# Kernel optimization log

Hardware: AMD Instinct MI355X
Metric: run time of the kernel (lower is better)

The kernel has to match this reference:

```python
import jax, jax.numpy as jnp
import numpy as np

N_HEADS = 16
HEAD_SIZE = 64
D_EMBD = 1024
BLOCK_SIZE = 1024
B, T = 4, 1024


def setup_inputs() -> dict:
    key = jax.random.key(0)
    ks = jax.random.split(key, 6)
    s = 0.02
    x = jax.random.normal(ks[0], (B, T, D_EMBD), dtype=jnp.float32)
    # per-head bias-free Q/K/V projections, stacked: [H, C, Hs]
    Wq = jax.random.normal(ks[1], (N_HEADS, D_EMBD, HEAD_SIZE), dtype=jnp.float32) * s
    Wk = jax.random.normal(ks[2], (N_HEADS, D_EMBD, HEAD_SIZE), dtype=jnp.float32) * s
    Wv = jax.random.normal(ks[3], (N_HEADS, D_EMBD, HEAD_SIZE), dtype=jnp.float32) * s
    # output projection W_o: Linear(d_embd, d_embd) with bias
    Wo = jax.random.normal(ks[4], (D_EMBD, D_EMBD), dtype=jnp.float32) * s
    bo = jax.random.normal(ks[5], (D_EMBD,), dtype=jnp.float32) * s
    return {"x": x, "Wq": Wq, "Wk": Wk, "Wv": Wv, "Wo": Wo, "bo": bo}


def reference(x, Wq, Wk, Wv, Wo, bo):
    # Batched equivalent of the per-head loop: q,k,v: [B, H, T, Hs]
    q = jnp.einsum('btc,hcs->bhts', x, Wq)
    k = jnp.einsum('btc,hcs->bhts', x, Wk)
    v = jnp.einsum('btc,hcs->bhts', x, Wv)
    scale = 1.0 / jnp.sqrt(jnp.asarray(HEAD_SIZE, dtype=x.dtype))
    scores = jnp.einsum('bhts,bhus->bhtu', q, k) * scale  # [B,H,T,T]
    causal = jnp.tril(jnp.ones((T, T), dtype=bool))
    scores = jnp.where(causal[None, None, :, :], scores, jnp.asarray(-jnp.inf, dtype=x.dtype))
    wei = jax.nn.softmax(scores, axis=-1)  # dropout p=0.0 -> identity
    out = jnp.einsum('bhtu,bhus->bhts', wei, v)  # [B,H,T,Hs]
    out = out.transpose(0, 2, 1, 3).reshape(B, T, D_EMBD)  # concat heads
    return out @ Wo.T + bo  # final Linear; dropout p=0.0 -> identity
```

## Files before the change

kernel.cpp:

```cpp
#include <hip/hip_runtime.h>
#include <hip/hip_bf16.h>
#include <math.h>

#define NH 16
#define HS 64
#define DE 1024
#define TT 1024
#define BBATCH 4
#define MTOK 4096

typedef __bf16 v8bf __attribute__((ext_vector_type(8)));
typedef __bf16 v4bf __attribute__((ext_vector_type(4)));
typedef float  v4f  __attribute__((ext_vector_type(4)));

__device__ __forceinline__ void gl_lds16(const __bf16* g, __bf16* l) {
    __builtin_amdgcn_global_load_lds(
        (const __attribute__((address_space(1))) unsigned int*)g,
        (__attribute__((address_space(3))) unsigned int*)l, 16, 0, 0);
}

__global__ __launch_bounds__(256) void prep_all_kernel(
    const float* __restrict__ x,  __bf16* __restrict__ xb,
    const float* __restrict__ Wo, __bf16* __restrict__ Wob,
    const float* __restrict__ Wq, const float* __restrict__ Wk,
    const float* __restrict__ Wv, __bf16* __restrict__ Wt)
{
    const int bid = blockIdx.x;
    const int t = threadIdx.x;
    if (bid < 5120) {
        int i = bid * 256 + t;
        const float* in; __bf16* out;
        if (i < 1048576) { in = x;  out = xb; }
        else             { in = Wo; out = Wob; i -= 1048576; }
        float4 v = ((const float4*)in)[i];
        v4bf o;
        o[0] = (__bf16)v.x; o[1] = (__bf16)v.y; o[2] = (__bf16)v.z; o[3] = (__bf16)v.w;
        *(v4bf*)&out[(size_t)i * 4] = o;
        return;
    }
    const int bid2 = bid - 5120;
    const int c0 = (bid2 & 15) * 64, h = (bid2 >> 4) & 15, m = bid2 >> 8;
    const float* W = (m == 0) ? Wq : (m == 1) ? Wk : Wv;
    __shared__ float tile[64][65];
    #pragma unroll
    for (int pp = 0; pp < 16; ++pp) {
        int cl = pp * 4 + (t >> 6);
        int s  = t & 63;
        tile[cl][s] = W[((size_t)h * DE + c0 + cl) * HS + s];
    }
    __syncthreads();
    #pragma unroll
    for (int pp = 0; pp < 16; ++pp) {
        int s  = pp * 4 + (t >> 6);
        int cl = t & 63;
        Wt[((size_t)(m * DE + h * HS + s)) * DE + c0 + cl] = (__bf16)tile[cl][s];
    }
}

__device__ __forceinline__ void gemm_stage(
    const __bf16* __restrict__ Ab, const __bf16* __restrict__ Bb,
    __bf16* As, __bf16* Bs, int K, int k0, int w, int l)
{
    #pragma unroll
    for (int i = 0; i < 4; ++i) {
        int p   = i * 256 + w * 64 + l;
        int row = p >> 3;
        int lc  = (p & 7) ^ (row & 7);
        gl_lds16(Ab + (size_t)row * K + k0 + lc * 8, As + p * 8);
        gl_lds16(Bb + (size_t)row * K + k0 + lc * 8, Bs + p * 8);
    }
}

__global__ __launch_bounds__(256) void gemm_bt_kernel(
    const __bf16* __restrict__ A, const __bf16* __restrict__ Bt,
    int K,
    __bf16* __restrict__ qk_out, __bf16* __restrict__ vt_out)
{
    __shared__ __align__(16) __bf16 As[128 * 64];
    __shared__ __align__(16) __bf16 Bs[128 * 64];
    const int tid = threadIdx.x;
    const int w = tid >> 6, l = tid & 63;
    const int wm = w >> 1, wn = w & 1;
    const int lhi = l >> 4, llo = l & 15;
    const int sw0 = ((lhi ^ (llo & 7)) << 3);
    const int sw1 = sw0 ^ 32;

    const int lin = blockIdx.x;
    const int xcd = lin & 7, j = lin >> 3;
    const int bm = xcd * 4 + (j & 3);
    const int bn = j >> 2;

    v4f acc[4][4];
    #pragma unroll
    for (int i = 0; i < 4; ++i)
        #pragma unroll
        for (int jj = 0; jj < 4; ++jj)
            #pragma unroll
            for (int r = 0; r < 4; ++r) acc[i][jj][r] = 0.f;

    const __bf16* Ab = A  + (size_t)bm * 128 * K;
    const __bf16* Bb = Bt + (size_t)bn * 128 * K;

    const int niter = K >> 6;
    for (int it = 0; it < niter; ++it) {
        if (it) __syncthreads();
        gemm_stage(Ab, Bb, As, Bs, K, it * 64, w, l);
        __syncthreads();
        #pragma unroll
        for (int kk = 0; kk < 64; kk += 32) {
            const int sw = kk ? sw1 : sw0;
            v8bf a[4], b[4];
            #pragma unroll
            for (int i = 0; i < 4; ++i)
                a[i] = *(const v8bf*)&As[(wm * 64 + i * 16 + llo) * 64 + sw];
            #pragma unroll
            for (int jj = 0; jj < 4; ++jj)
                b[jj] = *(const v8bf*)&Bs[(wn * 64 + jj * 16 + llo) * 64 + sw];
            #pragma unroll
            for (int i = 0; i < 4; ++i)
                #pragma unroll
                for (int jj = 0; jj < 4; ++jj)
                    acc[i][jj] = __builtin_amdgcn_mfma_f32_16x16x32_bf16(a[i], b[jj], acc[i][jj], 0, 0, 0);
        }
    }

    const int row0 = bm * 128 + wm * 64;
    const int col0 = bn * 128 + wn * 64;

    if (col0 < 2048) {
        #pragma unroll
        for (int i = 0; i < 4; ++i) {
            int rbase = row0 + i * 16 + lhi * 4;
            #pragma unroll
            for (int jj = 0; jj < 4; ++jj) {
                int c = col0 + jj * 16 + llo;
                #pragma unroll
                for (int r = 0; r < 4; ++r)
                    qk_out[(size_t)(rbase + r) * 2048 + c] = (__bf16)acc[i][jj][r];
            }
        }
    } else {
        #pragma unroll
        for (int i = 0; i < 4; ++i) {
            int rbase = row0 + i * 16 + lhi * 4;
            int bidx = rbase >> 10, t0 = rbase & 1023;
            #pragma unroll
            for (int jj = 0; jj < 4; ++jj) {
                int c = col0 + jj * 16 + llo - 2048;
                v4bf pk;
                #pragma unroll
                for (int r = 0; r < 4; ++r) pk[r] = (__bf16)acc[i][jj][r];
                *(v4bf*)&vt_out[((size_t)(bidx * NH + (c >> 6)) * HS + (c & 63)) * TT + t0] = pk;
            }
        }
    }
}

__global__ __launch_bounds__(256) void gemm_bt64_kernel(
    const __bf16* __restrict__ A, const __bf16* __restrict__ Bt, int K,
    float* __restrict__ f_out, const float* __restrict__ bias)
{
    __shared__ __align__(16) __bf16 As[2][64 * 64];
    __shared__ __align__(16) __bf16 Bs[2][128 * 64];
    const int tid = threadIdx.x;
    const int w = tid >> 6, l = tid & 63;
    const int wm = w & 1, wn = w >> 1;
    const int lhi = l >> 4, llo = l & 15;
    const int sw0 = ((lhi ^ (llo & 7)) << 3);
    const int sw1 = sw0 ^ 32;

    const int lin = blockIdx.x;
    const int xcd = lin & 7, j = lin >> 3;
    const int bm = xcd * 8 + (j & 7);
    const int bn = j >> 3;

    v4f acc[2][4];
    #pragma unroll
    for (int i = 0; i < 2; ++i)
        #pragma unroll
        for (int jj = 0; jj < 4; ++jj)
            #pragma unroll
            for (int r = 0; r < 4; ++r) acc[i][jj][r] = 0.f;

    const __bf16* Ab = A  + (size_t)bm * 64 * K;
    const __bf16* Bb = Bt + (size_t)bn * 128 * K;

    const int niter = K >> 6;
    {
        #pragma unroll
        for (int i = 0; i < 2; ++i) {
            int p = i * 256 + tid, row = p >> 3, lc = (p & 7) ^ (row & 7);
            gl_lds16(Ab + (size_t)row * K + lc * 8, As[0] + p * 8);
        }
        #pragma unroll
        for (int i = 0; i < 4; ++i) {
            int p = i * 256 + tid, row = p >> 3, lc = (p & 7) ^ (row & 7);
            gl_lds16(Bb + (size_t)row * K + lc * 8, Bs[0] + p * 8);
        }
    }

    for (int it = 0; it < niter; ++it) {
        const int buf = it & 1;
        __syncthreads();
        if (it + 1 < niter) {
            const int k0 = (it + 1) * 64;
            #pragma unroll
            for (int i = 0; i < 2; ++i) {
                int p = i * 256 + tid, row = p >> 3, lc = (p & 7) ^ (row & 7);
                gl_lds16(Ab + (size_t)row * K + k0 + lc * 8, As[buf ^ 1] + p * 8);
            }
            #pragma unroll
            for (int i = 0; i < 4; ++i) {
                int p = i * 256 + tid, row = p >> 3, lc = (p & 7) ^ (row & 7);
                gl_lds16(Bb + (size_t)row * K + k0 + lc * 8, Bs[buf ^ 1] + p * 8);
            }
        }
        #pragma unroll
        for (int kk = 0; kk < 64; kk += 32) {
            const int sw = kk ? sw1 : sw0;
            v8bf a[2], b[4];
            #pragma unroll
            for (int i = 0; i < 2; ++i)
                a[i] = *(const v8bf*)&As[buf][(wm * 32 + i * 16 + llo) * 64 + sw];
            #pragma unroll
            for (int jj = 0; jj < 4; ++jj)
                b[jj] = *(const v8bf*)&Bs[buf][(wn * 64 + jj * 16 + llo) * 64 + sw];
            #pragma unroll
            for (int i = 0; i < 2; ++i)
                #pragma unroll
                for (int jj = 0; jj < 4; ++jj)
                    acc[i][jj] = __builtin_amdgcn_mfma_f32_16x16x32_bf16(a[i], b[jj], acc[i][jj], 0, 0, 0);
        }
    }

    const int row0 = bm * 64 + wm * 32;
    const int col0 = bn * 128 + wn * 64;
    #pragma unroll
    for (int jj = 0; jj < 4; ++jj) {
        int c = col0 + jj * 16 + llo;
        float bv = bias[c];
        #pragma unroll
        for (int i = 0; i < 2; ++i) {
            int rbase = row0 + i * 16 + lhi * 4;
            #pragma unroll
            for (int r = 0; r < 4; ++r)
                f_out[(size_t)(rbase + r) * DE + c] = acc[i][jj][r] + bv;
        }
    }
}

__device__ __forceinline__ v4f bf_mfma(v8bf a, v8bf b, v4f c) {
    return __builtin_amdgcn_mfma_f32_16x16x32_bf16(a, b, c, 0, 0, 0);
}

__device__ __forceinline__ void stage_kv(
    const __bf16* __restrict__ kb, const __bf16* __restrict__ vb,
    __bf16* Ksb, __bf16* Vsb, int k0, int tid)
{
    #pragma unroll
    for (int i = 0; i < 2; ++i) {
        int p   = i * 256 + tid;
        int row = p >> 3;
        int lc  = (p & 7) ^ (row & 7);
        gl_lds16(kb + (size_t)(k0 + row) * 2048 + lc * 8, Ksb + p * 8);
        gl_lds16(vb + (size_t)row * TT + k0 + lc * 8,     Vsb + p * 8);
    }
}

template<bool DIAG>
__device__ __forceinline__ void attn_compute(
    const __bf16* __restrict__ Ksb, const __bf16* __restrict__ Vsb,
    __bf16* __restrict__ PsW, int k0, int r0, int lhi, int llo, int sw0, int sw1,
    v8bf aq0, v8bf aq1, v4f (&o)[4], float (&l_part)[4])
{
    v4f sacc[4];
    #pragma unroll
    for (int n = 0; n < 4; ++n)
        #pragma unroll
        for (int r = 0; r < 4; ++r) sacc[n][r] = 0.f;
    #pragma unroll
    for (int n = 0; n < 4; ++n) {
        v8bf bk0 = *(const v8bf*)&Ksb[(n * 16 + llo) * 64 + sw0];
        v8bf bk1 = *(const v8bf*)&Ksb[(n * 16 + llo) * 64 + sw1];
        sacc[n] = bf_mfma(aq0, bk0, sacc[n]);
        sacc[n] = bf_mfma(aq1, bk1, sacc[n]);
    }

    float prob[4][4];
    #pragma unroll
    for (int n = 0; n < 4; ++n) {
        int colg = k0 + n * 16 + llo;
        #pragma unroll
        for (int r = 0; r < 4; ++r) {
            float s2 = sacc[n][r] * 0.18033688f;
            if (DIAG) { int rowg = r0 + lhi * 4 + r; if (colg > rowg) s2 = -1e30f; }
            float p = exp2f(s2);
            prob[n][r] = p;
            l_part[r] += p;
        }
    }

    #pragma unroll
    for (int r = 0; r < 4; ++r) {
        int prow = lhi * 4 + r;
        #pragma unroll
        for (int n = 0; n < 4; ++n) {
            int g = (n * 2 + (llo >> 3)) ^ (prow & 7);
            PsW[prow * 64 + g * 8 + (llo & 7)] = (__bf16)prob[n][r];
        }
    }

    #pragma unroll
    for (int kk = 0; kk < 64; kk += 32) {
        v8bf ap = *(const v8bf*)&PsW[llo * 64 + (((kk >> 3) + lhi) ^ (llo & 7)) * 8];
        const int sw = kk ? sw1 : sw0;
        #pragma unroll
        for (int n = 0; n < 4; ++n) {
            v8bf bv = *(const v8bf*)&Vsb[(n * 16 + llo) * 64 + sw];
            o[n] = bf_mfma(ap, bv, o[n]);
        }
    }
}

__global__ __launch_bounds__(256) void attn_kernel(
    const __bf16* __restrict__ qk, const __bf16* __restrict__ vt,
    __bf16* __restrict__ att)
{
    __shared__ __align__(16) __bf16 Ks[2][64 * 64];
    __shared__ __align__(16) __bf16 Vs[2][64 * 64];
    __shared__ __align__(16) __bf16 Ps[4][16 * 64];

    const int tid = threadIdx.x;
    const int w = tid >> 6, l = tid & 63;
    const int lhi = l >> 4, llo = l & 15;
    const int sw0 = ((lhi ^ (llo & 7)) << 3);
    const int sw1 = sw0 ^ 32;
    const int bh = blockIdx.x & 63;
    const int k = blockIdx.x >> 6;
    const int qt = (k & 4) ? (k >= 12 ? k - 12 : k + 4) : (15 - k);
    const int b = bh >> 4, h = bh & 15;

    const __bf16* qbase = qk + (size_t)b * TT * 2048 + h * HS;
    const __bf16* kbase = qk + (size_t)b * TT * 2048 + 1024 + h * HS;
    const __bf16* vbase = vt + (size_t)bh * HS * TT;
    __bf16* PsW = &Ps[w][0];

    const int r0 = qt * 64 + w * 16;

    stage_kv(kbase, vbase, Ks[0], Vs[0], 0, tid);

    v8bf aq0 = *(const v8bf*)&qbase[(size_t)(r0 + llo) * 2048 + lhi * 8];
    v8bf aq1 = *(const v8bf*)&qbase[(size_t)(r0 + llo) * 2048 + 32 + lhi * 8];

    float l_part[4] = {0.f, 0.f, 0.f, 0.f};
    v4f o[4];
    #pragma unroll
    for (int n = 0; n < 4; ++n)
        #pragma unroll
        for (int r = 0; r < 4; ++r) o[n][r] = 0.f;

    for (int kt = 0; kt < qt; ++kt) {
        const int buf = kt & 1;
        __syncthreads();
        stage_kv(kbase, vbase, Ks[buf ^ 1], Vs[buf ^ 1], (kt + 1) * 64, tid);
        attn_compute<false>(Ks[buf], Vs[buf], PsW, kt * 64, r0, lhi, llo, sw0, sw1, aq0, aq1, o, l_part);
    }
    __syncthreads();
    attn_compute<true>(Ks[qt & 1], Vs[qt & 1], PsW, qt * 64, r0, lhi, llo, sw0, sw1, aq0, aq1, o, l_part);

    #pragma unroll
    for (int r = 0; r < 4; ++r) {
        float s = l_part[r];
        #pragma unroll
        for (int msk = 1; msk < 16; msk <<= 1) s += __shfl_xor(s, msk, 64);
        float inv = 1.f / s;
        int rowg = b * TT + r0 + lhi * 4 + r;
        #pragma unroll
        for (int n = 0; n < 4; ++n)
            att[(size_t)rowg * DE + h * HS + n * 16 + llo] = (__bf16)(o[n][r] * inv);
    }
}

extern "C" void kernel_launch(void* const* d_in, const int* in_sizes, int n_in,
                              void* d_out, int out_size, void* d_ws, size_t ws_size,
                              hipStream_t stream)
{
    const float* x  = (const float*)d_in[0];
    const float* Wq = (const float*)d_in[1];
    const float* Wk = (const float*)d_in[2];
    const float* Wv = (const float*)d_in[3];
    const float* Wo = (const float*)d_in[4];
    const float* bo = (const float*)d_in[5];
    float* out = (float*)d_out;

    char* ws = (char*)d_ws;
    __bf16* xb  = (__bf16*)(ws);
    __bf16* Wt  = (__bf16*)(ws + 8388608);
    __bf16* Wob = (__bf16*)(ws + 14680064);
    __bf16* qk  = (__bf16*)(ws + 16777216);
    __bf16* vt  = (__bf16*)(ws + 33554432);
    __bf16* att = (__bf16*)(ws + 41943040);

    prep_all_kernel<<<5888, 256, 0, stream>>>(x, xb, Wo, Wob, Wq, Wk, Wv, Wt);
    gemm_bt_kernel<<<768, 256, 0, stream>>>(xb, Wt, 1024, qk, vt);
    attn_kernel<<<1024, 256, 0, stream>>>(qk, vt, att);
    gemm_bt64_kernel<<<512, 256, 0, stream>>>(att, Wob, 1024, out, bo);
}
```

Measured before the change: 156.5 us.

## Replace QKV GEMM with 256x256 double-buffered 8-phase pipelined kernel

Replaces the 128x128 single-buffered QKV projection GEMM with a 512-thread kernel that computes 256x256 tiles. It double-buffers A and B in LDS and splits each K step into four phases. Global-to-LDS loads for the next step are interleaved with MFMA work, using explicit vmcnt waits, raw s_barrier calls and setprio. The goal is to hide load latency and raise data reuse per block. In exchange, only 192 blocks are launched and each needs 128KB of LDS, so fewer blocks than CUs and one block per CU.

```diff
diff --git a/kernel.cpp b/kernel.cpp
--- a/kernel.cpp
+++ b/kernel.cpp
@@ -17,6 +17,16 @@
     __builtin_amdgcn_global_load_lds(
         (const __attribute__((address_space(1))) unsigned int*)g,
         (__attribute__((address_space(3))) unsigned int*)l, 16, 0, 0);
+}
+
+__device__ __forceinline__ v4f bf_mfma(v8bf a, v8bf b, v4f c) {
+    return __builtin_amdgcn_mfma_f32_16x16x32_bf16(a, b, c, 0, 0, 0);
+}
+
+__device__ __forceinline__ void wg_barrier() {
+    asm volatile("" ::: "memory");
+    __builtin_amdgcn_s_barrier();
+    asm volatile("" ::: "memory");
 }
 
 __global__ __launch_bounds__(256) void prep_all_kernel(
@@ -57,99 +67,152 @@
     }
 }
 
-__device__ __forceinline__ void gemm_stage(
-    const __bf16* __restrict__ Ab, const __bf16* __restrict__ Bb,
-    __bf16* As, __bf16* Bs, int K, int k0, int w, int l)
-{
-    #pragma unroll
-    for (int i = 0; i < 4; ++i) {
-        int p   = i * 256 + w * 64 + l;
-        int row = p >> 3;
-        int lc  = (p & 7) ^ (row & 7);
-        gl_lds16(Ab + (size_t)row * K + k0 + lc * 8, As + p * 8);
-        gl_lds16(Bb + (size_t)row * K + k0 + lc * 8, Bs + p * 8);
-    }
-}
-
-__global__ __launch_bounds__(256) void gemm_bt_kernel(
+__device__ __forceinline__ void stage_half(
+    const __bf16* __restrict__ Gb, __bf16* Ls, int h, int k0, int tid)
+{
+    #pragma unroll
+    for (int i = 0; i < 2; ++i) {
+        int p  = i * 512 + tid;
+        int r  = p >> 3;
+        int lc = (p & 7) ^ (r & 7);
+        gl_lds16(Gb + (size_t)(h * 128 + r) * 1024 + k0 + lc * 8, Ls + h * 128 * 64 + p * 8);
+    }
+}
+
+__global__ __launch_bounds__(512, 2) void gemm_qkv_8ph(
     const __bf16* __restrict__ A, const __bf16* __restrict__ Bt,
-    int K,
     __bf16* __restrict__ qk_out, __bf16* __restrict__ vt_out)
 {
-    __shared__ __align__(16) __bf16 As[128 * 64];
-    __shared__ __align__(16) __bf16 Bs[128 * 64];
+    __shared__ __align__(16) __bf16 As[2][256 * 64];
+    __shared__ __align__(16) __bf16 Bs[2][256 * 64];
     const int tid = threadIdx.x;
     const int w = tid >> 6, l = tid & 63;
-    const int wm = w >> 1, wn = w & 1;
+    const int wm = w >> 2, wn = w & 3;
     const int lhi = l >> 4, llo = l & 15;
     const int sw0 = ((lhi ^ (llo & 7)) << 3);
     const int sw1 = sw0 ^ 32;
 
     const int lin = blockIdx.x;
-    const int xcd = lin & 7, j = lin >> 3;
-    const int bm = xcd * 4 + (j & 3);
-    const int bn = j >> 2;
-
-    v4f acc[4][4];
-    #pragma unroll
-    for (int i = 0; i < 4; ++i)
-        #pragma unroll
-        for (int jj = 0; jj < 4; ++jj)
-            #pragma unroll
-            for (int r = 0; r < 4; ++r) acc[i][jj][r] = 0.f;
-
-    const __bf16* Ab = A  + (size_t)bm * 128 * K;
-    const __bf16* Bb = Bt + (size_t)bn * 128 * K;
-
-    const int niter = K >> 6;
-    for (int it = 0; it < niter; ++it) {
-        if (it) __syncthreads();
-        gemm_stage(Ab, Bb, As, Bs, K, it * 64, w, l);
-        __syncthreads();
-        #pragma unroll
-        for (int kk = 0; kk < 64; kk += 32) {
-            const int sw = kk ? sw1 : sw0;
-            v8bf a[4], b[4];
-            #pragma unroll
-            for (int i = 0; i < 4; ++i)
-                a[i] = *(const v8bf*)&As[(wm * 64 + i * 16 + llo) * 64 + sw];
-            #pragma unroll
-            for (int jj = 0; jj < 4; ++jj)
-                b[jj] = *(const v8bf*)&Bs[(wn * 64 + jj * 16 + llo) * 64 + sw];
-            #pragma unroll
-            for (int i = 0; i < 4; ++i)
+    const int xcd = lin & 7, chunk = lin >> 3;
+    const int bm = xcd * 2 + (chunk & 1);
+    const int bn = chunk >> 1;
+
+    const __bf16* Ab = A  + (size_t)bm * 256 * 1024;
+    const __bf16* Bb = Bt + (size_t)bn * 256 * 1024;
+
+    v4f acc[8][4];
+    #pragma unroll
+    for (int fr = 0; fr < 8; ++fr)
+        #pragma unroll
+        for (int fc = 0; fc < 4; ++fc)
+            #pragma unroll
+            for (int r = 0; r < 4; ++r) acc[fr][fc][r] = 0.f;
+
+    stage_half(Ab, (__bf16*)As[0], 0, 0, tid);
+    stage_half(Ab, (__bf16*)As[0], 1, 0, tid);
+    stage_half(Bb, (__bf16*)Bs[0], 0, 0, tid);
+    stage_half(Bb, (__bf16*)Bs[0], 1, 0, tid);
+    stage_half(Ab, (__bf16*)As[1], 0, 64, tid);
+    stage_half(Ab, (__bf16*)As[1], 1, 64, tid);
+    stage_half(Bb, (__bf16*)Bs[1], 0, 64, tid);
+
+    #pragma unroll 1
+    for (int t = 0; t < 16; ++t) {
+        const __bf16* Ap = As[t & 1];
+        const __bf16* Bp = Bs[t & 1];
+        __bf16* Anx = (__bf16*)As[(t & 1) ^ 1];
+        __bf16* Bnx = (__bf16*)Bs[(t & 1) ^ 1];
+        const int knx = (t + 1) << 6;
+
+        if (t == 0)      stage_half(Bb, Bnx, 1, knx, tid);
+        else if (t < 15) stage_half(Ab, Anx, 0, knx, tid);
+
+        if (t == 0)      asm volatile("s_waitcnt vmcnt(6)" ::: "memory");
+        else if (t < 15) asm volatile("s_waitcnt vmcnt(2)" ::: "memory");
+        else             asm volatile("s_waitcnt vmcnt(0)" ::: "memory");
+        __builtin_amdgcn_sched_barrier(0);
+        wg_barrier();
+
+        v8bf bfr[4][2];
+        #pragma unroll
+        for (int fc = 0; fc < 4; ++fc) {
+            const int brow = wn * 64 + fc * 16 + llo;
+            bfr[fc][0] = *(const v8bf*)&Bp[brow * 64 + sw0];
+            bfr[fc][1] = *(const v8bf*)&Bp[brow * 64 + sw1];
+        }
+        {
+            v8bf afr[2][2];
+            #pragma unroll
+            for (int i = 0; i < 2; ++i) {
+                const int arow = wm * 128 + i * 16 + llo;
+                afr[i][0] = *(const v8bf*)&Ap[arow * 64 + sw0];
+                afr[i][1] = *(const v8bf*)&Ap[arow * 64 + sw1];
+            }
+            __builtin_amdgcn_s_setprio(1);
+            #pragma unroll
+            for (int i = 0; i < 2; ++i)
                 #pragma unroll
-                for (int jj = 0; jj < 4; ++jj)
-                    acc[i][jj] = __builtin_amdgcn_mfma_f32_16x16x32_bf16(a[i], b[jj], acc[i][jj], 0, 0, 0);
-        }
-    }
-
-    const int row0 = bm * 128 + wm * 64;
-    const int col0 = bn * 128 + wn * 64;
-
+                for (int fc = 0; fc < 4; ++fc) {
+                    acc[i][fc] = bf_mfma(afr[i][0], bfr[fc][0], acc[i][fc]);
+                    acc[i][fc] = bf_mfma(afr[i][1], bfr[fc][1], acc[i][fc]);
+                }
+            __builtin_amdgcn_s_setprio(0);
+        }
+        wg_barrier();
+
+        #pragma unroll
+        for (int q = 1; q < 4; ++q) {
+            v8bf afr[2][2];
+            #pragma unroll
+            for (int i = 0; i < 2; ++i) {
+                const int arow = wm * 128 + (q * 2 + i) * 16 + llo;
+                afr[i][0] = *(const v8bf*)&Ap[arow * 64 + sw0];
+                afr[i][1] = *(const v8bf*)&Ap[arow * 64 + sw1];
+            }
+            if (t >= 1 && t < 15) {
+                if (q == 1)      stage_half(Ab, Anx, 1, knx, tid);
+                else if (q == 2) stage_half(Bb, Bnx, 0, knx, tid);
+                else             stage_half(Bb, Bnx, 1, knx, tid);
+            }
+            wg_barrier();
+            __builtin_amdgcn_s_setprio(1);
+            #pragma unroll
+            for (int i = 0; i < 2; ++i)
+                #pragma unroll
+                for (int fc = 0; fc < 4; ++fc) {
+                    acc[q * 2 + i][fc] = bf_mfma(afr[i][0], bfr[fc][0], acc[q * 2 + i][fc]);
+                    acc[q * 2 + i][fc] = bf_mfma(afr[i][1], bfr[fc][1], acc[q * 2 + i][fc]);
+                }
+            __builtin_amdgcn_s_setprio(0);
+            wg_barrier();
+        }
+    }
+
+    const int row0 = bm * 256 + wm * 128;
+    const int col0 = bn * 256 + wn * 64;
     if (col0 < 2048) {
         #pragma unroll
-        for (int i = 0; i < 4; ++i) {
-            int rbase = row0 + i * 16 + lhi * 4;
-            #pragma unroll
-            for (int jj = 0; jj < 4; ++jj) {
-                int c = col0 + jj * 16 + llo;
+        for (int fr = 0; fr < 8; ++fr) {
+            const int rbase = row0 + fr * 16 + lhi * 4;
+            #pragma unroll
+            for (int fc = 0; fc < 4; ++fc) {
+                const int c = col0 + fc * 16 + llo;
                 #pragma unroll
                 for (int r = 0; r < 4; ++r)
-                    qk_out[(size_t)(rbase + r) * 2048 + c] = (__bf16)acc[i][jj][r];
+                    qk_out[(size_t)(rbase + r) * 2048 + c] = (__bf16)acc[fr][fc][r];
             }
         }
     } else {
         #pragma unroll
-        for (int i = 0; i < 4; ++i) {
-            int rbase = row0 + i * 16 + lhi * 4;
-            int bidx = rbase >> 10, t0 = rbase & 1023;
-            #pragma unroll
-            for (int jj = 0; jj < 4; ++jj) {
-                int c = col0 + jj * 16 + llo - 2048;
+        for (int fr = 0; fr < 8; ++fr) {
+            const int rbase = row0 + fr * 16 + lhi * 4;
+            const int bidx = rbase >> 10, t0 = rbase & 1023;
+            #pragma unroll
+            for (int fc = 0; fc < 4; ++fc) {
+                const int c = col0 + fc * 16 + llo - 2048;
                 v4bf pk;
                 #pragma unroll
-                for (int r = 0; r < 4; ++r) pk[r] = (__bf16)acc[i][jj][r];
+                for (int r = 0; r < 4; ++r) pk[r] = (__bf16)acc[fr][fc][r];
                 *(v4bf*)&vt_out[((size_t)(bidx * NH + (c >> 6)) * HS + (c & 63)) * TT + t0] = pk;
             }
         }
@@ -247,10 +310,6 @@
                 f_out[(size_t)(rbase + r) * DE + c] = acc[i][jj][r] + bv;
         }
     }
-}
-
-__device__ __forceinline__ v4f bf_mfma(v8bf a, v8bf b, v4f c) {
-    return __builtin_amdgcn_mfma_f32_16x16x32_bf16(a, b, c, 0, 0, 0);
 }
 
 __device__ __forceinline__ void stage_kv(
@@ -402,7 +461,7 @@
     __bf16* att = (__bf16*)(ws + 41943040);
 
     prep_all_kernel<<<5888, 256, 0, stream>>>(x, xb, Wo, Wob, Wq, Wk, Wv, Wt);
-    gemm_bt_kernel<<<768, 256, 0, stream>>>(xb, Wt, 1024, qk, vt);
+    gemm_qkv_8ph<<<192, 512, 0, stream>>>(xb, Wt, qk, vt);
     attn_kernel<<<1024, 256, 0, stream>>>(qk, vt, att);
     gemm_bt64_kernel<<<512, 256, 0, stream>>>(att, Wob, 1024, out, bo);
 }
```

New measurement: 169.2 us. 8.1% more time.

## Use 128x128 tiles with explicit waitcnt/barrier pipeline for output projection GEMM

Applied to the files above, without the earlier changes.

Replaces the 64x128 output-projection GEMM with a 128x128 tile kernel, where each wave computes a 64x64 sub-tile, and halves the grid to 256 blocks. Synchronisation changes to an explicit vmcnt wait plus a raw s_barrier after each stage instead of __syncthreads at the loop top. MFMA sections are wrapped in s_setprio. The goal is more data reuse per loaded byte and less barrier overhead, at the cost of fewer blocks (256 on a machine with 256 CUs) and higher register pressure.

```diff
diff --git a/kernel.cpp b/kernel.cpp
--- a/kernel.cpp
+++ b/kernel.cpp
@@ -17,6 +17,16 @@
     __builtin_amdgcn_global_load_lds(
         (const __attribute__((address_space(1))) unsigned int*)g,
         (__attribute__((address_space(3))) unsigned int*)l, 16, 0, 0);
+}
+
+__device__ __forceinline__ v4f bf_mfma(v8bf a, v8bf b, v4f c) {
+    return __builtin_amdgcn_mfma_f32_16x16x32_bf16(a, b, c, 0, 0, 0);
+}
+
+__device__ __forceinline__ void wg_barrier() {
+    asm volatile("" ::: "memory");
+    __builtin_amdgcn_s_barrier();
+    asm volatile("" ::: "memory");
 }
 
 __global__ __launch_bounds__(256) void prep_all_kernel(
@@ -156,101 +166,100 @@
     }
 }
 
-__global__ __launch_bounds__(256) void gemm_bt64_kernel(
-    const __bf16* __restrict__ A, const __bf16* __restrict__ Bt, int K,
+__device__ __forceinline__ void op_stage(
+    const __bf16* __restrict__ Ab, const __bf16* __restrict__ Bb,
+    __bf16* As, __bf16* Bs, int k0, int tid)
+{
+    #pragma unroll
+    for (int i = 0; i < 4; ++i) {
+        int p   = i * 256 + tid;
+        int row = p >> 3;
+        int lc  = (p & 7) ^ (row & 7);
+        gl_lds16(Ab + (size_t)row * 1024 + k0 + lc * 8, As + p * 8);
+        gl_lds16(Bb + (size_t)row * 1024 + k0 + lc * 8, Bs + p * 8);
+    }
+}
+
+__global__ __launch_bounds__(256) void gemm_op128_kernel(
+    const __bf16* __restrict__ A, const __bf16* __restrict__ Bt,
     float* __restrict__ f_out, const float* __restrict__ bias)
 {
-    __shared__ __align__(16) __bf16 As[2][64 * 64];
+    __shared__ __align__(16) __bf16 As[2][128 * 64];
     __shared__ __align__(16) __bf16 Bs[2][128 * 64];
     const int tid = threadIdx.x;
     const int w = tid >> 6, l = tid & 63;
-    const int wm = w & 1, wn = w >> 1;
+    const int wm = w >> 1, wn = w & 1;
     const int lhi = l >> 4, llo = l & 15;
     const int sw0 = ((lhi ^ (llo & 7)) << 3);
     const int sw1 = sw0 ^ 32;
 
     const int lin = blockIdx.x;
     const int xcd = lin & 7, j = lin >> 3;
-    const int bm = xcd * 8 + (j & 7);
-    const int bn = j >> 3;
-
-    v4f acc[2][4];
-    #pragma unroll
-    for (int i = 0; i < 2; ++i)
+    const int bm = xcd * 4 + (j & 3);
+    const int bn = j >> 2;
+
+    v4f acc[4][4];
+    #pragma unroll
+    for (int i = 0; i < 4; ++i)
         #pragma unroll
         for (int jj = 0; jj < 4; ++jj)
             #pragma unroll
             for (int r = 0; r < 4; ++r) acc[i][jj][r] = 0.f;
 
-    const __bf16* Ab = A  + (size_t)bm * 64 * K;
-    const __bf16* Bb = Bt + (size_t)bn * 128 * K;
-
-    const int niter = K >> 6;
-    {
-        #pragma unroll
-        for (int i = 0; i < 2; ++i) {
-            int p = i * 256 + tid, row = p >> 3, lc = (p & 7) ^ (row & 7);
-            gl_lds16(Ab + (size_t)row * K + lc * 8, As[0] + p * 8);
-        }
-        #pragma unroll
-        for (int i = 0; i < 4; ++i) {
-            int p = i * 256 + tid, row = p >> 3, lc = (p & 7) ^ (row & 7);
-            gl_lds16(Bb + (size_t)row * K + lc * 8, Bs[0] + p * 8);
-        }
-    }
-
-    for (int it = 0; it < niter; ++it) {
-        const int buf = it & 1;
-        __syncthreads();
-        if (it + 1 < niter) {
-            const int k0 = (it + 1) * 64;
-            #pragma unroll
-            for (int i = 0; i < 2; ++i) {
-                int p = i * 256 + tid, row = p >> 3, lc = (p & 7) ^ (row & 7);
-                gl_lds16(Ab + (size_t)row * K + k0 + lc * 8, As[buf ^ 1] + p * 8);
-            }
-            #pragma unroll
-            for (int i = 0; i < 4; ++i) {
-                int p = i * 256 + tid, row = p >> 3, lc = (p & 7) ^ (row & 7);
-                gl_lds16(Bb + (size_t)row * K + k0 + lc * 8, Bs[buf ^ 1] + p * 8);
-            }
-        }
+    const __bf16* Ab = A  + (size_t)bm * 128 * 1024;
+    const __bf16* Bb = Bt + (size_t)bn * 128 * 1024;
+
+    op_stage(Ab, Bb, (__bf16*)As[0], (__bf16*)Bs[0], 0, tid);
+    asm volatile("s_waitcnt vmcnt(0)" ::: "memory");
+    __builtin_amdgcn_sched_barrier(0);
+    wg_barrier();
+
+    #pragma unroll 1
+    for (int t = 0; t < 16; ++t) {
+        const int cur = t & 1;
+        if (t < 15)
+            op_stage(Ab, Bb, (__bf16*)As[cur ^ 1], (__bf16*)Bs[cur ^ 1], (t + 1) * 64, tid);
+
         #pragma unroll
         for (int kk = 0; kk < 64; kk += 32) {
             const int sw = kk ? sw1 : sw0;
-            v8bf a[2], b[4];
-            #pragma unroll
-            for (int i = 0; i < 2; ++i)
-                a[i] = *(const v8bf*)&As[buf][(wm * 32 + i * 16 + llo) * 64 + sw];
+            v8bf a[4], b[4];
+            #pragma unroll
+            for (int i = 0; i < 4; ++i)
+                a[i] = *(const v8bf*)&As[cur][(wm * 64 + i * 16 + llo) * 64 + sw];
             #pragma unroll
             for (int jj = 0; jj < 4; ++jj)
-                b[jj] = *(const v8bf*)&Bs[buf][(wn * 64 + jj * 16 + llo) * 64 + sw];
-            #pragma unroll
-            for (int i = 0; i < 2; ++i)
+                b[jj] = *(const v8bf*)&Bs[cur][(wn * 64 + jj * 16 + llo) * 64 + sw];
+            __builtin_amdgcn_s_setprio(1);
+            #pragma unroll
+            for (int i = 0; i < 4; ++i)
                 #pragma unroll
                 for (int jj = 0; jj < 4; ++jj)
-                    acc[i][jj] = __builtin_amdgcn_mfma_f32_16x16x32_bf16(a[i], b[jj], acc[i][jj], 0, 0, 0);
-        }
-    }
-
-    const int row0 = bm * 64 + wm * 32;
+                    acc[i][jj] = bf_mfma(a[i], b[jj], acc[i][jj]);
+            __builtin_amdgcn_s_setprio(0);
+        }
+
+        if (t < 15) {
+            asm volatile("s_waitcnt vmcnt(0)" ::: "memory");
+            __builtin_amdgcn_sched_barrier(0);
+            wg_barrier();
+        }
+    }
+
+    const int row0 = bm * 128 + wm * 64;
     const int col0 = bn * 128 + wn * 64;
     #pragma unroll
     for (int jj = 0; jj < 4; ++jj) {
         int c = col0 + jj * 16 + llo;
         float bv = bias[c];
         #pragma unroll
-        for (int i = 0; i < 2; ++i) {
+        for (int i = 0; i < 4; ++i) {
             int rbase = row0 + i * 16 + lhi * 4;
             #pragma unroll
             for (int r = 0; r < 4; ++r)
                 f_out[(size_t)(rbase + r) * DE + c] = acc[i][jj][r] + bv;
         }
     }
-}
-
-__device__ __forceinline__ v4f bf_mfma(v8bf a, v8bf b, v4f c) {
-    return __builtin_amdgcn_mfma_f32_16x16x32_bf16(a, b, c, 0, 0, 0);
 }
 
 __device__ __forceinline__ void stage_kv(
@@ -404,5 +413,5 @@
     prep_all_kernel<<<5888, 256, 0, stream>>>(x, xb, Wo, Wob, Wq, Wk, Wv, Wt);
     gemm_bt_kernel<<<768, 256, 0, stream>>>(xb, Wt, 1024, qk, vt);
     attn_kernel<<<1024, 256, 0, stream>>>(qk, vt, att);
-    gemm_bt64_kernel<<<512, 256, 0, stream>>>(att, Wob, 1024, out, bo);
-}
+    gemm_op128_kernel<<<256, 256, 0, stream>>>(att, Wob, out, bo);
+}
```

New measurement: 158.3 us. Within noise of the previous version (+1.1%).
